# Kernel tuning notes

Measured on AMD Instinct MI355X. Metric: run time of the kernel, lower is better.

Reference implementation:

```python
import jax, jax.numpy as jnp
import numpy as np

MAX_DISTANCE = 10
SCALE = 0.01

def distance_bias(seq_len):
    # |i - j| clamped to MAX_DISTANCE, scaled
    idx = jnp.arange(seq_len, dtype=jnp.float32)
    d = jnp.abs(idx[None, :] - idx[:, None])
    return jnp.clip(d, 0.0, MAX_DISTANCE) * SCALE  # [S, S]

def setup_inputs() -> dict:
    key = jax.random.key(0)
    k1, k2 = jax.random.split(key)
    B, S, D_IN, D_OUT = 8, 2048, 1024, 1024
    x = jax.random.normal(k1, (B, S, D_IN), dtype=jnp.float32)
    W = jax.random.normal(k2, (D_IN, D_OUT), dtype=jnp.float32) * (1.0 / np.sqrt(D_IN))
    b = jnp.zeros((D_OUT,), dtype=jnp.float32)
    return {"x": x, "W": W, "b": b}

def reference(x, W, b):
    B, S, _ = x.shape
    f = x @ W + b                                   # [B, S, H]
    e = jnp.einsum('bsd,btd->bst', f, f)            # scores [B, S, S]
    e = e + distance_bias(S)[None, :, :]
    a = jax.nn.softmax(e, axis=-1)
    out = jnp.einsum('bst,btd->bsd', a, f)          # weighted sum [B, S, H]
    return out
```

## Files before the change

kernel.cpp:

```cpp
#include <hip/hip_runtime.h>
#include <hip/hip_bf16.h>
#include <stdint.h>

typedef __attribute__((ext_vector_type(8))) short bf16x8;
typedef __attribute__((ext_vector_type(4))) float f32x4;
typedef unsigned short ushort_t;

static __device__ __forceinline__ unsigned short f2bf(float f) {
  union { float f; unsigned int u; } v; v.f = f;
  unsigned int u = v.u;
  u += 0x7FFFu + ((u >> 16) & 1u);
  return (unsigned short)(u >> 16);
}
static __device__ __forceinline__ float bf2f(unsigned short h) {
  union { unsigned int u; float f; } v; v.u = ((unsigned int)h) << 16; return v.f;
}

typedef __attribute__((address_space(1))) void gvoid;
typedef __attribute__((address_space(3))) void lvoid;
static __device__ __forceinline__ void gload_lds16(const void* gp, void* lp) {
  __builtin_amdgcn_global_load_lds((gvoid*)gp, (lvoid*)lp, 16, 0, 0);
}

__global__ __launch_bounds__(256) void k_convX(const float* __restrict__ X,
                                               unsigned short* __restrict__ Xb) {
  size_t i = ((size_t)blockIdx.x * 256 + threadIdx.x) * 8;
  const size_t stride = (size_t)4096 * 256 * 8;
  for (; i < (size_t)16777216; i += stride) {
    float4 v0 = *(const float4*)(X + i), v1 = *(const float4*)(X + i + 4);
    unsigned short h[8];
    h[0]=f2bf(v0.x); h[1]=f2bf(v0.y); h[2]=f2bf(v0.z); h[3]=f2bf(v0.w);
    h[4]=f2bf(v1.x); h[5]=f2bf(v1.y); h[6]=f2bf(v1.z); h[7]=f2bf(v1.w);
    *(uint4*)(Xb + i) = *(uint4*)h;
  }
}

__global__ __launch_bounds__(256) void k_convW(const float* __restrict__ W,
                                               unsigned short* __restrict__ Wt) {
  __shared__ __align__(16) unsigned short lds[64][72];
  const int tid = threadIdx.x;
  const int n0 = blockIdx.x * 64, k0 = blockIdx.y * 64;
  for (int i = 0; i < 4; ++i) {
    int c = i * 256 + tid;
    int r = c >> 4, c4 = (c & 15) * 4;
    float4 v = *(const float4*)(W + (size_t)(k0 + r) * 1024 + n0 + c4);
    unsigned short* p = &lds[r][c4];
    p[0] = f2bf(v.x); p[1] = f2bf(v.y); p[2] = f2bf(v.z); p[3] = f2bf(v.w);
  }
  __syncthreads();
  for (int i = 0; i < 2; ++i) {
    int c = i * 256 + tid;
    int n = c >> 3, k8 = (c & 7) * 8;
    unsigned short tmp[8];
    for (int j = 0; j < 8; ++j) tmp[j] = lds[k8 + j][n];
    *(uint4*)(Wt + (size_t)(n0 + n) * 1024 + k0 + k8) = *(uint4*)tmp;
  }
}

__global__ __launch_bounds__(256) void k_transF(const unsigned short* __restrict__ F,
                                                unsigned short* __restrict__ Ft) {
  __shared__ __align__(16) unsigned short lds[64][72];
  const int tid = threadIdx.x;
  const int t0 = blockIdx.x * 64, d0 = blockIdx.y * 64;
  const unsigned short* Fb = F + (size_t)blockIdx.z * 2048 * 1024;
  unsigned short* Ftb = Ft + (size_t)blockIdx.z * 1024 * 2048;
  for (int i = 0; i < 2; ++i) {
    int c = i * 256 + tid;
    int r = c >> 3, d8 = (c & 7) * 8;
    *(uint4*)(&lds[r][d8]) = *(const uint4*)(Fb + (size_t)(t0 + r) * 1024 + d0 + d8);
  }
  __syncthreads();
  for (int i = 0; i < 2; ++i) {
    int c = i * 256 + tid;
    int d = c >> 3, t8 = (c & 7) * 8;
    unsigned short tmp[8];
    for (int j = 0; j < 8; ++j) tmp[j] = lds[t8 + j][d];
    *(uint4*)(Ftb + (size_t)(d0 + d) * 2048 + t0 + t8) = *(uint4*)tmp;
  }
}


#define GEMM_PREAMBLE                                                         \
  const int tid = threadIdx.x, lane = tid & 63, wid = tid >> 6;               \
  const int wr = wid >> 2, wc = wid & 3;                                      \
  const int rl = lane & 15, k8 = (lane >> 4) * 8;                             \
  f32x4 acc[8][4] = {};

#define STAGE_ONE(dst, src, ld, row0, kcol0)                                  \
  _Pragma("unroll") for (int r_ = 0; r_ < 2; ++r_) {                          \
    int chunk_ = r_ * 8 + wid;                                                \
    gload_lds16((src) + (size_t)((row0) + chunk_ * 16 + (lane >> 2)) * (ld)   \
                      + (kcol0) + (lane & 3) * 8,                             \
                (char*)(dst) + chunk_ * 1024);                                \
  }

#define COMPUTE_TILE(Abuf, Bbuf)                                              \
  {                                                                           \
    bf16x8 a_[8], b_[4];                                                      \
    _Pragma("unroll") for (int m_ = 0; m_ < 8; ++m_)                          \
      a_[m_] = *(const bf16x8*)((Abuf) + (wr * 128 + m_ * 16 + rl) * 32 + k8);\
    _Pragma("unroll") for (int n_ = 0; n_ < 4; ++n_)                          \
      b_[n_] = *(const bf16x8*)((Bbuf) + (wc * 64 + n_ * 16 + rl) * 32 + k8); \
    _Pragma("unroll") for (int m_ = 0; m_ < 8; ++m_)                          \
      _Pragma("unroll") for (int n_ = 0; n_ < 4; ++n_)                        \
        acc[m_][n_] = __builtin_amdgcn_mfma_f32_16x16x32_bf16(                \
            a_[m_], b_[n_], acc[m_][n_], 0, 0, 0);                            \
  }

#define GEMM_MAIN(Asrc, Alda, arow0, Bsrc, Blda, brow0, NT)                   \
  __shared__ __align__(16) unsigned short As[2][8192];                        \
  __shared__ __align__(16) unsigned short Bs[2][8192];                        \
  STAGE_ONE(As[0], Asrc, Alda, arow0, 0)                                      \
  STAGE_ONE(Bs[0], Bsrc, Blda, brow0, 0)                                      \
  __syncthreads();                                                            \
  int cur = 0;                                                                \
  for (int t = 0; t < (NT) - 1; ++t) {                                        \
    STAGE_ONE(As[cur ^ 1], Asrc, Alda, arow0, (t + 1) * 32)                   \
    STAGE_ONE(Bs[cur ^ 1], Bsrc, Blda, brow0, (t + 1) * 32)                   \
    COMPUTE_TILE(As[cur], Bs[cur])                                            \
    __syncthreads();                                                          \
    cur ^= 1;                                                                 \
  }                                                                           \
  COMPUTE_TILE(As[cur], Bs[cur])

__global__ __launch_bounds__(512, 2) void k_gemm1(const unsigned short* __restrict__ Xb,
                                                  const unsigned short* __restrict__ Wt,
                                                  const float* __restrict__ bias,
                                                  unsigned short* __restrict__ F) {
  const int bid = blockIdx.x;
  const int swz = (bid & 7) * 32 + (bid >> 3);
  const int m0 = (swz >> 2) * 256, n0 = (swz & 3) * 256;
  GEMM_PREAMBLE
  GEMM_MAIN(Xb, 1024, m0, Wt, 1024, n0, 32)
  const int r4 = (lane >> 4) * 4, cl = lane & 15;
#pragma unroll
  for (int n = 0; n < 4; ++n) {
    int col = n0 + wc * 64 + n * 16 + cl;
    float bv = bias[col];
#pragma unroll
    for (int m = 0; m < 8; ++m) {
      int row = m0 + wr * 128 + m * 16 + r4;
#pragma unroll
      for (int j = 0; j < 4; ++j)
        F[(size_t)(row + j) * 1024 + col] = f2bf(acc[m][n][j] + bv);
    }
  }
}

__global__ __launch_bounds__(512, 2) void k_gemm2(const unsigned short* __restrict__ F,
                                                  unsigned short* __restrict__ E) {
  const int bid = blockIdx.x;
  const int swz = (bid & 7) * 64 + (bid >> 3);
  const int z = swz >> 6;
  const int m0 = ((swz >> 3) & 7) * 256, n0 = (swz & 7) * 256;
  const unsigned short* Fb = F + (size_t)z * 2048 * 1024;
  unsigned short* Eb = E + (size_t)z * 2048 * 2048;
  GEMM_PREAMBLE
  GEMM_MAIN(Fb, 1024, m0, Fb, 1024, n0, 32)
  const int r4 = (lane >> 4) * 4, cl = lane & 15;
#pragma unroll
  for (int m = 0; m < 8; ++m) {
    int row = m0 + wr * 128 + m * 16 + r4;
#pragma unroll
    for (int n = 0; n < 4; ++n) {
      int col = n0 + wc * 64 + n * 16 + cl;
#pragma unroll
      for (int j = 0; j < 4; ++j) {
        int rr = row + j;
        int d = rr - col; d = d < 0 ? -d : d; d = d > 10 ? 10 : d;
        Eb[(size_t)rr * 2048 + col] = f2bf(acc[m][n][j] + (float)d * 0.01f);
      }
    }
  }
}

__global__ __launch_bounds__(256) void k_softmax(unsigned short* __restrict__ E) {
  unsigned short* row = E + (size_t)blockIdx.x * 2048;
  const int tid = threadIdx.x, lane = tid & 63, w = tid >> 6;
  uint4 v = *(const uint4*)(row + tid * 8);
  float f[8];
  const unsigned int* up = (const unsigned int*)&v;
  for (int i = 0; i < 4; ++i) {
    f[2*i]   = bf2f((unsigned short)(up[i] & 0xFFFF));
    f[2*i+1] = bf2f((unsigned short)(up[i] >> 16));
  }
  float mx = f[0];
  for (int i = 1; i < 8; ++i) mx = fmaxf(mx, f[i]);
  for (int s = 32; s > 0; s >>= 1) mx = fmaxf(mx, __shfl_xor(mx, s));
  __shared__ float redm[4], reds[4];
  if (lane == 0) redm[w] = mx;
  __syncthreads();
  mx = fmaxf(fmaxf(redm[0], redm[1]), fmaxf(redm[2], redm[3]));
  float p[8], sum = 0.f;
  for (int i = 0; i < 8; ++i) { p[i] = __expf(f[i] - mx); sum += p[i]; }
  for (int s = 32; s > 0; s >>= 1) sum += __shfl_xor(sum, s);
  if (lane == 0) reds[w] = sum;
  __syncthreads();
  sum = reds[0] + reds[1] + reds[2] + reds[3];
  float inv = 1.0f / sum;
  unsigned short h[8];
  for (int i = 0; i < 8; ++i) h[i] = f2bf(p[i] * inv);
  *(uint4*)(row + tid * 8) = *(uint4*)h;
}

__global__ __launch_bounds__(512, 2) void k_gemm3(const unsigned short* __restrict__ P,
                                                  const unsigned short* __restrict__ Ft,
                                                  float* __restrict__ out) {
  const int bid = blockIdx.x;
  const int swz = (bid & 7) * 32 + (bid >> 3);
  const int z = swz >> 5;
  const int m0 = ((swz >> 2) & 7) * 256, n0 = (swz & 3) * 256;
  const unsigned short* Pb = P + (size_t)z * 2048 * 2048;
  const unsigned short* Ftb = Ft + (size_t)z * 1024 * 2048;
  float* outb = out + (size_t)z * 2048 * 1024;
  GEMM_PREAMBLE
  GEMM_MAIN(Pb, 2048, m0, Ftb, 2048, n0, 64)
  const int r4 = (lane >> 4) * 4, cl = lane & 15;
#pragma unroll
  for (int m = 0; m < 8; ++m) {
    int row = m0 + wr * 128 + m * 16 + r4;
#pragma unroll
    for (int n = 0; n < 4; ++n) {
      int col = n0 + wc * 64 + n * 16 + cl;
#pragma unroll
      for (int j = 0; j < 4; ++j)
        outb[(size_t)(row + j) * 1024 + col] = acc[m][n][j];
    }
  }
}

extern "C" void kernel_launch(void* const* d_in, const int* in_sizes, int n_in,
                              void* d_out, int out_size, void* d_ws, size_t ws_size,
                              hipStream_t stream) {
  const float* x = (const float*)d_in[0];
  const float* W = (const float*)d_in[1];
  const float* b = (const float*)d_in[2];
  float* out = (float*)d_out;

  unsigned short* Wt = (unsigned short*)d_ws;
  unsigned short* F  = (unsigned short*)((char*)d_ws + (2ull   << 20));
  unsigned short* Ft = (unsigned short*)((char*)d_ws + (34ull  << 20));
  unsigned short* E  = (unsigned short*)((char*)d_ws + (66ull  << 20));
  unsigned short* Xb = (unsigned short*)((char*)d_ws + (130ull << 20));

  k_convW  <<<dim3(16, 16),    256, 0, stream>>>(W, Wt);
  k_convX  <<<dim3(4096),      256, 0, stream>>>(x, Xb);
  k_gemm1  <<<dim3(256),       512, 0, stream>>>(Xb, Wt, b, F);
  k_transF <<<dim3(32, 16, 8), 256, 0, stream>>>(F, Ft);
  k_gemm2  <<<dim3(512),       512, 0, stream>>>(F, E);
  k_softmax<<<dim3(16384),     256, 0, stream>>>(E);
  k_gemm3  <<<dim3(256),       512, 0, stream>>>(E, Ft, out);
}
```

Measured before the change: 383.6 us.

## Deepen GEMM pipeline to 4-stage ring with swizzled LDS and split MFMA phases

Replaces the double-buffered GEMM macro with a templated core that keeps a 4-slot LDS ring, prefetching three k-tiles ahead and gating on explicit vmcnt waits. LDS staging and reads use an XOR-swizzled column slot to avoid bank conflicts, and each k-step is split into two MFMA halves interleaved with the next global-to-LDS loads, using setprio around MFMA. LDS use grows to 128KB per block, which likely drops occupancy from two blocks per CU to one, and the many raw barriers and waitcnts make correctness depend on exact ordering.

```diff
diff --git a/kernel.cpp b/kernel.cpp
--- a/kernel.cpp
+++ b/kernel.cpp
@@ -4,7 +4,6 @@
 
 typedef __attribute__((ext_vector_type(8))) short bf16x8;
 typedef __attribute__((ext_vector_type(4))) float f32x4;
-typedef unsigned short ushort_t;
 
 static __device__ __forceinline__ unsigned short f2bf(float f) {
   union { float f; unsigned int u; } v; v.f = f;
@@ -80,58 +79,91 @@
 }
 
 
-#define GEMM_PREAMBLE                                                         \
-  const int tid = threadIdx.x, lane = tid & 63, wid = tid >> 6;               \
-  const int wr = wid >> 2, wc = wid & 3;                                      \
-  const int rl = lane & 15, k8 = (lane >> 4) * 8;                             \
-  f32x4 acc[8][4] = {};
-
-#define STAGE_ONE(dst, src, ld, row0, kcol0)                                  \
-  _Pragma("unroll") for (int r_ = 0; r_ < 2; ++r_) {                          \
-    int chunk_ = r_ * 8 + wid;                                                \
-    gload_lds16((src) + (size_t)((row0) + chunk_ * 16 + (lane >> 2)) * (ld)   \
-                      + (kcol0) + (lane & 3) * 8,                             \
-                (char*)(dst) + chunk_ * 1024);                                \
-  }
-
-#define COMPUTE_TILE(Abuf, Bbuf)                                              \
-  {                                                                           \
-    bf16x8 a_[8], b_[4];                                                      \
-    _Pragma("unroll") for (int m_ = 0; m_ < 8; ++m_)                          \
-      a_[m_] = *(const bf16x8*)((Abuf) + (wr * 128 + m_ * 16 + rl) * 32 + k8);\
-    _Pragma("unroll") for (int n_ = 0; n_ < 4; ++n_)                          \
-      b_[n_] = *(const bf16x8*)((Bbuf) + (wc * 64 + n_ * 16 + rl) * 32 + k8); \
-    _Pragma("unroll") for (int m_ = 0; m_ < 8; ++m_)                          \
-      _Pragma("unroll") for (int n_ = 0; n_ < 4; ++n_)                        \
-        acc[m_][n_] = __builtin_amdgcn_mfma_f32_16x16x32_bf16(                \
-            a_[m_], b_[n_], acc[m_][n_], 0, 0, 0);                            \
-  }
-
-#define GEMM_MAIN(Asrc, Alda, arow0, Bsrc, Blda, brow0, NT)                   \
-  __shared__ __align__(16) unsigned short As[2][8192];                        \
-  __shared__ __align__(16) unsigned short Bs[2][8192];                        \
-  STAGE_ONE(As[0], Asrc, Alda, arow0, 0)                                      \
-  STAGE_ONE(Bs[0], Bsrc, Blda, brow0, 0)                                      \
-  __syncthreads();                                                            \
-  int cur = 0;                                                                \
-  for (int t = 0; t < (NT) - 1; ++t) {                                        \
-    STAGE_ONE(As[cur ^ 1], Asrc, Alda, arow0, (t + 1) * 32)                   \
-    STAGE_ONE(Bs[cur ^ 1], Bsrc, Blda, brow0, (t + 1) * 32)                   \
-    COMPUTE_TILE(As[cur], Bs[cur])                                            \
-    __syncthreads();                                                          \
-    cur ^= 1;                                                                 \
-  }                                                                           \
-  COMPUTE_TILE(As[cur], Bs[cur])
+template<int NT>
+__device__ __forceinline__ void gemm_core(
+    const unsigned short* __restrict__ Ag, int lda, int ar0,
+    const unsigned short* __restrict__ Bg, int ldb, int br0,
+    unsigned short* __restrict__ As, unsigned short* __restrict__ Bs,
+    f32x4 (&acc)[8][4]) {
+  const int tid = threadIdx.x, lane = tid & 63, wid = tid >> 6;
+  const int wr = wid >> 2, wc = wid & 3;
+  const int rl = lane & 15;
+  const int rslot = (((lane >> 4) ^ (lane & 3) ^ ((lane >> 2) & 3))) * 8;
+  const int q = tid >> 2;
+  const int sslot = (((tid & 3) ^ (q & 3) ^ ((q >> 2) & 3))) * 8;
+
+#define STAGE_T(dstbase, src, ld, r0, kt)                                      \
+  _Pragma("unroll")                                                            \
+  for (int r_ = 0; r_ < 2; ++r_)                                               \
+    gload_lds16((src) + (size_t)((r0) + r_ * 128 + q) * (ld) + (kt) * 32 + sslot, \
+                (char*)(dstbase) + r_ * 8192 + wid * 1024);
+
+  STAGE_T(As + 0 * 8192, Ag, lda, ar0, 0)
+  STAGE_T(Bs + 0 * 8192, Bg, ldb, br0, 0)
+  STAGE_T(As + 1 * 8192, Ag, lda, ar0, 1)
+  STAGE_T(Bs + 1 * 8192, Bg, ldb, br0, 1)
+  STAGE_T(As + 2 * 8192, Ag, lda, ar0, 2)
+  STAGE_T(Bs + 2 * 8192, Bg, ldb, br0, 2)
+  asm volatile("s_waitcnt vmcnt(8)" ::: "memory");
+  __builtin_amdgcn_s_barrier();
+
+  bf16x8 a[4], b[4], a2[4];
+  for (int t = 0; t < NT; ++t) {
+    const int sl = t & 3;
+    const int ps = (t + 3 < NT) ? (t + 3) : (NT - 1);
+    const int psl = (t + 3) & 3;
+    const unsigned short* Ab = As + sl * 8192;
+    const unsigned short* Bb = Bs + sl * 8192;
+#pragma unroll
+    for (int m = 0; m < 4; ++m)
+      a[m] = *(const bf16x8*)(Ab + (wr * 128 + m * 16 + rl) * 32 + rslot);
+#pragma unroll
+    for (int n = 0; n < 4; ++n)
+      b[n] = *(const bf16x8*)(Bb + (wc * 64 + n * 16 + rl) * 32 + rslot);
+    STAGE_T(As + psl * 8192, Ag, lda, ar0, ps)
+    __builtin_amdgcn_s_barrier();
+    asm volatile("s_waitcnt lgkmcnt(0)" ::: "memory");
+    __builtin_amdgcn_s_setprio(1);
+#pragma unroll
+    for (int m = 0; m < 4; ++m)
+#pragma unroll
+      for (int n = 0; n < 4; ++n)
+        acc[m][n] = __builtin_amdgcn_mfma_f32_16x16x32_bf16(a[m], b[n], acc[m][n], 0, 0, 0);
+    __builtin_amdgcn_s_setprio(0);
+    __builtin_amdgcn_s_barrier();
+#pragma unroll
+    for (int m = 0; m < 4; ++m)
+      a2[m] = *(const bf16x8*)(Ab + (wr * 128 + (m + 4) * 16 + rl) * 32 + rslot);
+    STAGE_T(Bs + psl * 8192, Bg, ldb, br0, ps)
+    __builtin_amdgcn_s_barrier();
+    asm volatile("s_waitcnt lgkmcnt(0)" ::: "memory");
+    __builtin_amdgcn_s_setprio(1);
+#pragma unroll
+    for (int m = 0; m < 4; ++m)
+#pragma unroll
+      for (int n = 0; n < 4; ++n)
+        acc[m + 4][n] = __builtin_amdgcn_mfma_f32_16x16x32_bf16(a2[m], b[n], acc[m + 4][n], 0, 0, 0);
+    __builtin_amdgcn_s_setprio(0);
+    asm volatile("s_waitcnt vmcnt(8)" ::: "memory");
+    __builtin_amdgcn_s_barrier();
+  }
+  asm volatile("s_waitcnt vmcnt(0)" ::: "memory");
+#undef STAGE_T
+}
 
 __global__ __launch_bounds__(512, 2) void k_gemm1(const unsigned short* __restrict__ Xb,
                                                   const unsigned short* __restrict__ Wt,
                                                   const float* __restrict__ bias,
                                                   unsigned short* __restrict__ F) {
+  __shared__ __align__(16) unsigned short As[4 * 8192];
+  __shared__ __align__(16) unsigned short Bs[4 * 8192];
   const int bid = blockIdx.x;
   const int swz = (bid & 7) * 32 + (bid >> 3);
   const int m0 = (swz >> 2) * 256, n0 = (swz & 3) * 256;
-  GEMM_PREAMBLE
-  GEMM_MAIN(Xb, 1024, m0, Wt, 1024, n0, 32)
+  f32x4 acc[8][4] = {};
+  gemm_core<32>(Xb, 1024, m0, Wt, 1024, n0, As, Bs, acc);
+  const int tid = threadIdx.x, lane = tid & 63, wid = tid >> 6;
+  const int wr = wid >> 2, wc = wid & 3;
   const int r4 = (lane >> 4) * 4, cl = lane & 15;
 #pragma unroll
   for (int n = 0; n < 4; ++n) {
@@ -149,14 +181,18 @@
 
 __global__ __launch_bounds__(512, 2) void k_gemm2(const unsigned short* __restrict__ F,
                                                   unsigned short* __restrict__ E) {
+  __shared__ __align__(16) unsigned short As[4 * 8192];
+  __shared__ __align__(16) unsigned short Bs[4 * 8192];
   const int bid = blockIdx.x;
   const int swz = (bid & 7) * 64 + (bid >> 3);
   const int z = swz >> 6;
   const int m0 = ((swz >> 3) & 7) * 256, n0 = (swz & 7) * 256;
   const unsigned short* Fb = F + (size_t)z * 2048 * 1024;
   unsigned short* Eb = E + (size_t)z * 2048 * 2048;
-  GEMM_PREAMBLE
-  GEMM_MAIN(Fb, 1024, m0, Fb, 1024, n0, 32)
+  f32x4 acc[8][4] = {};
+  gemm_core<32>(Fb, 1024, m0, Fb, 1024, n0, As, Bs, acc);
+  const int tid = threadIdx.x, lane = tid & 63, wid = tid >> 6;
+  const int wr = wid >> 2, wc = wid & 3;
   const int r4 = (lane >> 4) * 4, cl = lane & 15;
 #pragma unroll
   for (int m = 0; m < 8; ++m) {
@@ -206,6 +242,8 @@
 __global__ __launch_bounds__(512, 2) void k_gemm3(const unsigned short* __restrict__ P,
                                                   const unsigned short* __restrict__ Ft,
                                                   float* __restrict__ out) {
+  __shared__ __align__(16) unsigned short As[4 * 8192];
+  __shared__ __align__(16) unsigned short Bs[4 * 8192];
   const int bid = blockIdx.x;
   const int swz = (bid & 7) * 32 + (bid >> 3);
   const int z = swz >> 5;
@@ -213,8 +251,10 @@
   const unsigned short* Pb = P + (size_t)z * 2048 * 2048;
   const unsigned short* Ftb = Ft + (size_t)z * 1024 * 2048;
   float* outb = out + (size_t)z * 2048 * 1024;
-  GEMM_PREAMBLE
-  GEMM_MAIN(Pb, 2048, m0, Ftb, 2048, n0, 64)
+  f32x4 acc[8][4] = {};
+  gemm_core<64>(Pb, 2048, m0, Ftb, 2048, n0, As, Bs, acc);
+  const int tid = threadIdx.x, lane = tid & 63, wid = tid >> 6;
+  const int wr = wid >> 2, wc = wid & 3;
   const int r4 = (lane >> 4) * 4, cl = lane & 15;
 #pragma unroll
   for (int m = 0; m < 8; ++m) {
```

New measurement: 353.6 us. -7.8%, faster.
